# Kernel tuning notes

Measured on AMD Instinct MI355X. Metric: run time of the kernel, lower is better.

The kernel has to match this reference:

```python
import jax, jax.numpy as jnp
import numpy as np


def setup_inputs() -> dict:
    key = jax.random.key(0)
    k1, k2 = jax.random.split(key)
    B, L, D = 16, 2048, 1024
    sentout = jax.random.normal(k1, (B, L, D), dtype=jnp.float32)
    nl_input = jax.random.randint(k2, (B, L), 0, 4, dtype=jnp.int64)
    return {"sentout": sentout, "nl_input": nl_input}


def reference(sentout, nl_input):
    # Per batch row: stable partition of sentout rows -- positions where
    # nl_input != 0 first (in original order), then positions where == 0.
    # Equivalent to tf.gather_nd(where(!=0)) ++ tf.gather_nd(where(==0)).
    # A stable argsort on the key (is_padding: 0 for facts, 1 for pads)
    # produces exactly this permutation, fully vectorized over the batch.
    is_pad = (nl_input == 0).astype(jnp.int32)          # [B, L]
    order = jnp.argsort(is_pad, axis=1, stable=True)    # [B, L]
    # Gather encoded facts in the partitioned order: [B, L, D]
    return jnp.take_along_axis(sentout, order[:, :, None], axis=1)
```

## Files before the change

kernel.cpp:

```cpp
#include <hip/hip_runtime.h>

constexpr int L_CONST = 2048;
constexpr int D_CONST = 1024;
constexpr int SCAN_T  = 256;
constexpr int PER     = L_CONST / SCAN_T;

__global__ __launch_bounds__(SCAN_T) void build_order_kernel(
    const int* __restrict__ nl, int* __restrict__ order) {
    const int b = blockIdx.x;
    const int t = threadIdx.x;
    const int* row = nl + (size_t)b * L_CONST;

    int flags[PER];
    int cnt = 0;
    #pragma unroll
    for (int k = 0; k < PER; ++k) {
        int v = row[t * PER + k];
        flags[k] = (v != 0) ? 1 : 0;
        cnt += flags[k];
    }

    __shared__ int s[SCAN_T];
    s[t] = cnt;
    __syncthreads();
    #pragma unroll
    for (int off = 1; off < SCAN_T; off <<= 1) {
        int add = (t >= off) ? s[t - off] : 0;
        __syncthreads();
        s[t] += add;
        __syncthreads();
    }
    const int incl     = s[t];
    const int totalNon = s[SCAN_T - 1];
    const int exclNon  = incl - cnt;

    int run = 0;
    #pragma unroll
    for (int k = 0; k < PER; ++k) {
        const int j        = t * PER + k;
        const int npPrefix = exclNon + run;
        int dest;
        if (flags[k]) dest = npPrefix;
        else          dest = totalNon + (j - npPrefix);
        order[(size_t)b * L_CONST + dest] = j;
        run += flags[k];
    }
}

__global__ __launch_bounds__(256) void gather_kernel(
    const float* __restrict__ in, const int* __restrict__ order,
    float* __restrict__ out) {
    constexpr int D4 = D_CONST / 4;
    const int bi  = blockIdx.x;
    const int b   = bi >> 11;
    const int src = order[bi];
    const float4* srcp = (const float4*)in  + ((size_t)b * L_CONST + src) * D4;
    float4*       dstp = (float4*)out       + (size_t)bi * D4;
    dstp[threadIdx.x] = srcp[threadIdx.x];
}

extern "C" void kernel_launch(void* const* d_in, const int* in_sizes, int n_in,
                              void* d_out, int out_size, void* d_ws, size_t ws_size,
                              hipStream_t stream) {
    const float* sentout = (const float*)d_in[0];
    const int*   nl      = (const int*)d_in[1];
    float*       out     = (float*)d_out;
    int*         order   = (int*)d_ws;

    const int B = in_sizes[1] / L_CONST;

    build_order_kernel<<<B, SCAN_T, 0, stream>>>(nl, order);
    gather_kernel<<<B * L_CONST, 256, 0, stream>>>(sentout, order, out);
}
```

Before: 47.66 us.

## Fuse partition scan into gather with per-block redundant scan and 16-row tiles

Merges the order-building scan and the row gather into one kernel. Each block recomputes the per-row stable partition in shared memory and then copies 16 output rows. This removes the serial 16-block scan kernel, the workspace round trip and a launch. In exchange every block repeats the full 2048-element scan and its barriers.

```diff
diff --git a/kernel.cpp b/kernel.cpp
--- a/kernel.cpp
+++ b/kernel.cpp
@@ -2,36 +2,44 @@
 
 constexpr int L_CONST = 2048;
 constexpr int D_CONST = 1024;
-constexpr int SCAN_T  = 256;
-constexpr int PER     = L_CONST / SCAN_T;
+constexpr int NT      = 256;
+constexpr int PER     = L_CONST / NT;
+constexpr int ROWS    = 16;
+constexpr int GROUPS  = L_CONST / ROWS;
+constexpr int D4      = D_CONST / 4;
 
-__global__ __launch_bounds__(SCAN_T) void build_order_kernel(
-    const int* __restrict__ nl, int* __restrict__ order) {
-    const int b = blockIdx.x;
+__global__ __launch_bounds__(NT) void fused_partition_gather(
+    const float* __restrict__ in, const int* __restrict__ nl,
+    float* __restrict__ out) {
+    const int b = blockIdx.x / GROUPS;
+    const int g = blockIdx.x % GROUPS;
     const int t = threadIdx.x;
-    const int* row = nl + (size_t)b * L_CONST;
 
+    const int4* row4 = (const int4*)(nl + (size_t)b * L_CONST);
+    int4 v0 = row4[t * 2];
+    int4 v1 = row4[t * 2 + 1];
     int flags[PER];
+    flags[0] = (v0.x != 0); flags[1] = (v0.y != 0);
+    flags[2] = (v0.z != 0); flags[3] = (v0.w != 0);
+    flags[4] = (v1.x != 0); flags[5] = (v1.y != 0);
+    flags[6] = (v1.z != 0); flags[7] = (v1.w != 0);
     int cnt = 0;
     #pragma unroll
-    for (int k = 0; k < PER; ++k) {
-        int v = row[t * PER + k];
-        flags[k] = (v != 0) ? 1 : 0;
-        cnt += flags[k];
-    }
+    for (int k = 0; k < PER; ++k) cnt += flags[k];
 
-    __shared__ int s[SCAN_T];
+    __shared__ int s[NT];
+    __shared__ int lds_order[L_CONST];
     s[t] = cnt;
     __syncthreads();
     #pragma unroll
-    for (int off = 1; off < SCAN_T; off <<= 1) {
+    for (int off = 1; off < NT; off <<= 1) {
         int add = (t >= off) ? s[t - off] : 0;
         __syncthreads();
         s[t] += add;
         __syncthreads();
     }
     const int incl     = s[t];
-    const int totalNon = s[SCAN_T - 1];
+    const int totalNon = s[NT - 1];
     const int exclNon  = incl - cnt;
 
     int run = 0;
@@ -39,24 +47,22 @@
     for (int k = 0; k < PER; ++k) {
         const int j        = t * PER + k;
         const int npPrefix = exclNon + run;
-        int dest;
-        if (flags[k]) dest = npPrefix;
-        else          dest = totalNon + (j - npPrefix);
-        order[(size_t)b * L_CONST + dest] = j;
+        const int dest = flags[k] ? npPrefix : (totalNon + (j - npPrefix));
+        lds_order[dest] = j;
         run += flags[k];
     }
-}
+    __syncthreads();
 
-__global__ __launch_bounds__(256) void gather_kernel(
-    const float* __restrict__ in, const int* __restrict__ order,
-    float* __restrict__ out) {
-    constexpr int D4 = D_CONST / 4;
-    const int bi  = blockIdx.x;
-    const int b   = bi >> 11;
-    const int src = order[bi];
-    const float4* srcp = (const float4*)in  + ((size_t)b * L_CONST + src) * D4;
-    float4*       dstp = (float4*)out       + (size_t)bi * D4;
-    dstp[threadIdx.x] = srcp[threadIdx.x];
+    int srcs[ROWS];
+    #pragma unroll
+    for (int r = 0; r < ROWS; ++r) srcs[r] = lds_order[g * ROWS + r];
+
+    const float4* inb  = (const float4*)in  + (size_t)b * L_CONST * D4;
+    float4*       outb = (float4*)out       + ((size_t)b * L_CONST + (size_t)g * ROWS) * D4;
+    #pragma unroll
+    for (int r = 0; r < ROWS; ++r) {
+        outb[r * D4 + t] = inb[(size_t)srcs[r] * D4 + t];
+    }
 }
 
 extern "C" void kernel_launch(void* const* d_in, const int* in_sizes, int n_in,
@@ -65,10 +71,7 @@
     const float* sentout = (const float*)d_in[0];
     const int*   nl      = (const int*)d_in[1];
     float*       out     = (float*)d_out;
-    int*         order   = (int*)d_ws;
 
     const int B = in_sizes[1] / L_CONST;
-
-    build_order_kernel<<<B, SCAN_T, 0, stream>>>(nl, order);
-    gather_kernel<<<B * L_CONST, 256, 0, stream>>>(sentout, order, out);
+    fused_partition_gather<<<B * GROUPS, NT, 0, stream>>>(sentout, nl, out);
 }
```

Measured after the change: 47.27 us. No clear change (-0.8%).
